# Kernel optimization log

Measured on AMD Instinct MI355X. Metric: run time of the kernel, lower is better.

The kernel has to match this reference:

```python
import jax, jax.numpy as jnp
import numpy as np

GRID = 8          # proto_grid
EPS = 1e-4        # safe_norm eps
TAU = 20.0        # temperature used throughout


def avg_pool(x, k):
    # non-overlapping avg pool, kernel k divides H and W exactly
    S, C, H, W = x.shape
    return x.reshape(S, C, H // k, k, W // k, k).mean(axis=(3, 5))


def safe_norm(x, axis):
    n = jnp.sqrt(jnp.sum(x * x, axis=axis, keepdims=True))
    return x / jnp.maximum(n, EPS)


def setup_inputs() -> dict:
    key = jax.random.key(0)
    k1, k2, k3 = jax.random.split(key, 3)
    qry = jax.random.normal(k1, (1, 1, 256, 128, 128), dtype=jnp.float32)
    sup_x = jax.random.normal(k2, (1, 5, 1, 256, 128, 128), dtype=jnp.float32)
    sup_y = jax.random.uniform(k3, (1, 5, 1, 128, 128), dtype=jnp.float32)
    return {"qry": qry, "sup_x": sup_x, "sup_y": sup_y, "thresh": 0}


def reference(qry, sup_x, sup_y, thresh):
    # mode == 'gridconv', use_cross_attn=False, isval=False
    qry = qry[:, 0]          # squeeze(1)        -> [1, 256, 128, 128]
    sup_x = sup_x[0, :, 0]   # squeeze(0,2)      -> [5, 256, 128, 128]
    sup_y = sup_y[0]         # squeeze(0)        -> [5, 1, 128, 128]

    shot, nc, H, W = sup_x.shape
    k = H // GRID

    # grid prototypes: avgpool then [shot, nc, g*g] -> [shot, g*g, nc] -> [shot*g*g, nc]
    n_sup = avg_pool(sup_x, k)
    protos = n_sup.reshape(shot, nc, -1).transpose(0, 2, 1).reshape(-1, nc)
    # selection mask: avg_pool(sup_y) > thresh. sup_y is uniform(0,1) and
    # thresh=0, so every grid cell is selected -> selection is the identity
    # (fixed-shape, jit-safe; matches the torch boolean index exactly here).

    # mean-center then safe L2-normalize (channel dim)
    protos = protos - protos.mean(axis=-1, keepdims=True)
    qryc = qry - qry.mean(axis=1, keepdims=True)
    pro_n = safe_norm(protos, axis=1)        # [npro, nc]
    qry_n = safe_norm(qryc, axis=1)          # [b, nc, h, w]

    # 1x1 conv as cosine similarity against prototype bank
    dists = jnp.einsum('bchw,pc->bphw', qry_n, pro_n) * TAU   # [b, npro, h, w]
    prob = jax.nn.softmax(dists, axis=1)
    # bmm combine: channel-wise weighted prototypes per pixel
    ch_proto = jnp.einsum('pc,bphw->bchw', pro_n, prob)       # [b, nc, h, w]
    pred_grid = jnp.sum(qry_n * ch_proto * TAU, axis=1, keepdims=True)

    debug_assign = jnp.argmax(dists, axis=1).astype(jnp.float32)
    return pred_grid, debug_assign
```

## Files before the change

### kernel.cpp

```cpp
#include <hip/hip_runtime.h>

#define NCH   256
#define NPROT 320
#define HW    16384
#define TAU   20.0f
#define EPSN  1e-4f

__global__ __launch_bounds__(256) void k_pool(const float* __restrict__ sup_x,
                                              float* __restrict__ praw) {
    int b = blockIdx.x;
    int t = threadIdx.x;
    const float4* plane = (const float4*)(sup_x + (size_t)b * HW);
    float rsum[8];
    #pragma unroll
    for (int r = 0; r < 8; ++r) rsum[r] = 0.f;
    #pragma unroll
    for (int i = 0; i < 16; ++i) {
        float4 v = plane[i * 256 + t];
        rsum[i >> 1] += v.x + v.y + v.z + v.w;
    }
    __shared__ float part[8][256];
    #pragma unroll
    for (int r = 0; r < 8; ++r) part[r][t] = rsum[r];
    __syncthreads();
    int R  = t >> 5;
    int cw = t & 31;
    float s = 0.f;
    #pragma unroll
    for (int a = 0; a < 8; ++a) s += part[R][a * 32 + cw];
    s += __shfl_xor(s, 1);
    s += __shfl_xor(s, 2);
    if ((t & 3) == 0) {
        int shot = b >> 8, c = b & 255;
        int p = shot * 64 + R * 8 + (cw >> 2);
        praw[(size_t)p * NCH + c] = s * (1.0f / 256.0f);
    }
}

__device__ __forceinline__ float block_sum256(float x, float* ws4, int t) {
    #pragma unroll
    for (int o = 1; o < 64; o <<= 1) x += __shfl_xor(x, o);
    if ((t & 63) == 0) ws4[t >> 6] = x;
    __syncthreads();
    float r = ws4[0] + ws4[1] + ws4[2] + ws4[3];
    __syncthreads();
    return r;
}

__global__ __launch_bounds__(256) void k_norm(const float* __restrict__ praw,
                                              float* __restrict__ PT,
                                              float* __restrict__ sp) {
    int p = blockIdx.x;
    int c = threadIdx.x;
    __shared__ float ws4[4];
    float v = praw[p * NCH + c];
    float mean = block_sum256(v, ws4, c) * (1.0f / 256.0f);
    float cen = v - mean;
    float n2 = block_sum256(cen * cen, ws4, c);
    float inv = 1.0f / fmaxf(sqrtf(n2), EPSN);
    float pn = cen * inv;
    PT[(size_t)(c >> 2) * NPROT * 4 + p * 4 + (c & 3)] = pn;
    float ssum = block_sum256(pn, ws4, c);
    if (c == 0) sp[p] = ssum;
}

__global__ __launch_bounds__(256, 2) void k_main(const float* __restrict__ qry,
                                                 const float* __restrict__ PT,
                                                 const float* __restrict__ sp,
                                                 float* __restrict__ out) {
    __shared__ __align__(16) float smem[9472];
    __shared__ float meanv[32], invnv[32];
    int t = threadIdx.x;
    int pixbase = blockIdx.x * 32;

    {
        int f4 = t & 7;
        int c0 = t >> 3;
        #pragma unroll
        for (int i = 0; i < 8; ++i) {
            int c = c0 + 32 * i;
            float4 v = *(const float4*)(qry + (size_t)c * HW + pixbase + f4 * 4);
            int px = f4 * 4;
            smem[(px + 0) * 260 + c] = v.x;
            smem[(px + 1) * 260 + c] = v.y;
            smem[(px + 2) * 260 + c] = v.z;
            smem[(px + 3) * 260 + c] = v.w;
        }
    }
    __syncthreads();

    {
        int pix = t & 31, sub = t >> 5;
        float s1 = 0.f, s2 = 0.f;
        #pragma unroll
        for (int j = 0; j < 32; ++j) {
            float q = smem[pix * 260 + sub * 32 + j];
            s1 += q; s2 += q * q;
        }
        smem[8320 + sub * 32 + pix] = s1;
        smem[8576 + sub * 32 + pix] = s2;
    }
    __syncthreads();
    if (t < 32) {
        float s1 = 0.f, s2 = 0.f;
        #pragma unroll
        for (int j = 0; j < 8; ++j) { s1 += smem[8320 + j * 32 + t]; s2 += smem[8576 + j * 32 + t]; }
        float mean = s1 * (1.0f / 256.0f);
        float n2 = fmaxf(s2 - s1 * mean, 0.f);
        meanv[t] = mean;
        invnv[t] = 1.0f / fmaxf(sqrtf(n2), EPSN);
    }
    __syncthreads();

    int lane = t & 63;
    int w = t >> 6;
    float acc[8][5];
    #pragma unroll
    for (int i = 0; i < 8; ++i)
        #pragma unroll
        for (int j = 0; j < 5; ++j) acc[i][j] = 0.f;

    {
        const float4* pptr = (const float4*)PT + lane;
        const float* qbase = smem + w * 8 * 260;
        for (int cb = 0; cb < 64; ++cb) {
            float4 pv0 = pptr[0];
            float4 pv1 = pptr[64];
            float4 pv2 = pptr[128];
            float4 pv3 = pptr[192];
            float4 pv4 = pptr[256];
            #pragma unroll
            for (int i = 0; i < 8; ++i) {
                float4 qv = *(const float4*)(qbase + i * 260);
                acc[i][0] = fmaf(qv.x, pv0.x, acc[i][0]);
                acc[i][0] = fmaf(qv.y, pv0.y, acc[i][0]);
                acc[i][0] = fmaf(qv.z, pv0.z, acc[i][0]);
                acc[i][0] = fmaf(qv.w, pv0.w, acc[i][0]);
                acc[i][1] = fmaf(qv.x, pv1.x, acc[i][1]);
                acc[i][1] = fmaf(qv.y, pv1.y, acc[i][1]);
                acc[i][1] = fmaf(qv.z, pv1.z, acc[i][1]);
                acc[i][1] = fmaf(qv.w, pv1.w, acc[i][1]);
                acc[i][2] = fmaf(qv.x, pv2.x, acc[i][2]);
                acc[i][2] = fmaf(qv.y, pv2.y, acc[i][2]);
                acc[i][2] = fmaf(qv.z, pv2.z, acc[i][2]);
                acc[i][2] = fmaf(qv.w, pv2.w, acc[i][2]);
                acc[i][3] = fmaf(qv.x, pv3.x, acc[i][3]);
                acc[i][3] = fmaf(qv.y, pv3.y, acc[i][3]);
                acc[i][3] = fmaf(qv.z, pv3.z, acc[i][3]);
                acc[i][3] = fmaf(qv.w, pv3.w, acc[i][3]);
                acc[i][4] = fmaf(qv.x, pv4.x, acc[i][4]);
                acc[i][4] = fmaf(qv.y, pv4.y, acc[i][4]);
                acc[i][4] = fmaf(qv.z, pv4.z, acc[i][4]);
                acc[i][4] = fmaf(qv.w, pv4.w, acc[i][4]);
            }
            pptr += NPROT;
            qbase += 4;
        }
    }

    float spv[5];
    #pragma unroll
    for (int j = 0; j < 5; ++j) spv[j] = sp[lane + 64 * j];

    float m8[8], S8[8], T8[8], I8[8];
    #pragma unroll
    for (int i = 0; i < 8; ++i) {
        int pix = w * 8 + i;
        float mean = meanv[pix], invn = invnv[pix];
        float d[5];
        float m = -1e30f; int bj = 0;
        #pragma unroll
        for (int j = 0; j < 5; ++j) {
            d[j] = TAU * invn * (acc[i][j] - mean * spv[j]);
            if (d[j] > m) { m = d[j]; bj = j; }
        }
        float S = 0.f, T = 0.f;
        #pragma unroll
        for (int j = 0; j < 5; ++j) {
            float e = __expf(d[j] - m);
            S += e; T += e * d[j];
        }
        m8[i] = m; S8[i] = S; T8[i] = T; I8[i] = (float)(lane + 64 * bj);
    }
    __syncthreads();

    float* M  = smem;
    float* Sa = smem + 2080;
    float* Ta = smem + 4160;
    float* Ia = smem + 6240;
    #pragma unroll
    for (int i = 0; i < 8; ++i) {
        int pix = w * 8 + i;
        M [pix * 65 + lane] = m8[i];
        Sa[pix * 65 + lane] = S8[i];
        Ta[pix * 65 + lane] = T8[i];
        Ia[pix * 65 + lane] = I8[i];
    }
    __syncthreads();

    float* P2m = smem + 8320;
    float* P2s = smem + 8608;
    float* P2t = smem + 8896;
    float* P2i = smem + 9184;
    {
        int pix = t >> 3, oct = t & 7;
        int base = pix * 65 + oct * 8;
        float gm = -1e30f;
        #pragma unroll
        for (int k = 0; k < 8; ++k) gm = fmaxf(gm, M[base + k]);
        float S = 0.f, T = 0.f, bi = 0.f, bm = -1e30f;
        #pragma unroll
        for (int k = 0; k < 8; ++k) {
            float mk = M[base + k];
            float wg = __expf(mk - gm);
            S += Sa[base + k] * wg;
            T += Ta[base + k] * wg;
            if (mk > bm) { bm = mk; bi = Ia[base + k]; }
        }
        P2m[pix * 9 + oct] = gm;
        P2s[pix * 9 + oct] = S;
        P2t[pix * 9 + oct] = T;
        P2i[pix * 9 + oct] = bi;
    }
    __syncthreads();

    if (t < 32) {
        float gm = -1e30f;
        #pragma unroll
        for (int k = 0; k < 8; ++k) gm = fmaxf(gm, P2m[t * 9 + k]);
        float S = 0.f, T = 0.f, bi = 0.f, bm = -1e30f;
        #pragma unroll
        for (int k = 0; k < 8; ++k) {
            float mk = P2m[t * 9 + k];
            float wg = __expf(mk - gm);
            S += P2s[t * 9 + k] * wg;
            T += P2t[t * 9 + k] * wg;
            if (mk > bm) { bm = mk; bi = P2i[t * 9 + k]; }
        }
        out[pixbase + t] = T / S;
        out[HW + pixbase + t] = bi;
    }
}

extern "C" void kernel_launch(void* const* d_in, const int* in_sizes, int n_in,
                              void* d_out, int out_size, void* d_ws, size_t ws_size,
                              hipStream_t stream) {
    const float* qry   = (const float*)d_in[0];
    const float* sup_x = (const float*)d_in[1];
    float* out = (float*)d_out;

    float* praw = (float*)d_ws;
    float* PT   = praw + NPROT * NCH;
    float* sp   = PT + NPROT * NCH;

    k_pool<<<5 * 256, 256, 0, stream>>>(sup_x, praw);
    k_norm<<<NPROT, 256, 0, stream>>>(praw, PT, sp);
    k_main<<<HW / 32, 256, 0, stream>>>(qry, PT, sp, out);
}
```

Measured before the change: 192.9 us.

## Compute prototype similarity with split-fp16 MFMA instead of scalar FP32 FMAs

Moves the query-prototype dot product from scalar FP32 FMA loops onto 16x16x32 fp16 MFMA instructions. Both operands are split into fp16 hi and scaled lo parts, and three MFMA products recover near-FP32 accuracy. Queries are normalized and split in LDS with an XOR swizzle, and prototypes are stored pre-split in k_norm, so the sum-of-prototype correction term goes away. The softmax/argmax reduction is restructured around the MFMA output layout using shuffles and a smaller cross-wave combine. This adds conversion work and LDS usage, and risks small precision differences.

```diff
diff --git a/kernel.cpp b/kernel.cpp
--- a/kernel.cpp
+++ b/kernel.cpp
@@ -5,6 +5,9 @@
 #define HW    16384
 #define TAU   20.0f
 #define EPSN  1e-4f
+
+typedef _Float16 half8 __attribute__((ext_vector_type(8)));
+typedef float    f32x4 __attribute__((ext_vector_type(4)));
 
 __global__ __launch_bounds__(256) void k_pool(const float* __restrict__ sup_x,
                                               float* __restrict__ praw) {
@@ -48,8 +51,8 @@
 }
 
 __global__ __launch_bounds__(256) void k_norm(const float* __restrict__ praw,
-                                              float* __restrict__ PT,
-                                              float* __restrict__ sp) {
+                                              _Float16* __restrict__ PTh,
+                                              _Float16* __restrict__ PTl) {
     int p = blockIdx.x;
     int c = threadIdx.x;
     __shared__ float ws4[4];
@@ -59,17 +62,23 @@
     float n2 = block_sum256(cen * cen, ws4, c);
     float inv = 1.0f / fmaxf(sqrtf(n2), EPSN);
     float pn = cen * inv;
-    PT[(size_t)(c >> 2) * NPROT * 4 + p * 4 + (c & 3)] = pn;
-    float ssum = block_sum256(pn, ws4, c);
-    if (c == 0) sp[p] = ssum;
+    _Float16 hi = (_Float16)pn;
+    float lo = (pn - (float)hi) * 2048.0f;
+    size_t idx = ((size_t)(c >> 3) * NPROT + p) * 8 + (c & 7);
+    PTh[idx] = hi;
+    PTl[idx] = (_Float16)lo;
 }
 
 __global__ __launch_bounds__(256, 2) void k_main(const float* __restrict__ qry,
-                                                 const float* __restrict__ PT,
-                                                 const float* __restrict__ sp,
+                                                 const _Float16* __restrict__ PTh,
+                                                 const _Float16* __restrict__ PTl,
                                                  float* __restrict__ out) {
-    __shared__ __align__(16) float smem[9472];
+    __shared__ __align__(16) float qlds[32 * 260];
+    __shared__ float red[512];
+    __shared__ __align__(16) _Float16 Ah[32 * 256];
+    __shared__ __align__(16) _Float16 Al[32 * 256];
     __shared__ float meanv[32], invnv[32];
+    __shared__ float Mw[4][32], Sw[4][32], Tw[4][32], Iw[4][32];
     int t = threadIdx.x;
     int pixbase = blockIdx.x * 32;
 
@@ -81,10 +90,10 @@
             int c = c0 + 32 * i;
             float4 v = *(const float4*)(qry + (size_t)c * HW + pixbase + f4 * 4);
             int px = f4 * 4;
-            smem[(px + 0) * 260 + c] = v.x;
-            smem[(px + 1) * 260 + c] = v.y;
-            smem[(px + 2) * 260 + c] = v.z;
-            smem[(px + 3) * 260 + c] = v.w;
+            qlds[(px + 0) * 260 + c] = v.x;
+            qlds[(px + 1) * 260 + c] = v.y;
+            qlds[(px + 2) * 260 + c] = v.z;
+            qlds[(px + 3) * 260 + c] = v.w;
         }
     }
     __syncthreads();
@@ -94,17 +103,17 @@
         float s1 = 0.f, s2 = 0.f;
         #pragma unroll
         for (int j = 0; j < 32; ++j) {
-            float q = smem[pix * 260 + sub * 32 + j];
+            float q = qlds[pix * 260 + sub * 32 + j];
             s1 += q; s2 += q * q;
         }
-        smem[8320 + sub * 32 + pix] = s1;
-        smem[8576 + sub * 32 + pix] = s2;
+        red[sub * 32 + pix] = s1;
+        red[256 + sub * 32 + pix] = s2;
     }
     __syncthreads();
     if (t < 32) {
         float s1 = 0.f, s2 = 0.f;
         #pragma unroll
-        for (int j = 0; j < 8; ++j) { s1 += smem[8320 + j * 32 + t]; s2 += smem[8576 + j * 32 + t]; }
+        for (int j = 0; j < 8; ++j) { s1 += red[j * 32 + t]; s2 += red[256 + j * 32 + t]; }
         float mean = s1 * (1.0f / 256.0f);
         float n2 = fmaxf(s2 - s1 * mean, 0.f);
         meanv[t] = mean;
@@ -112,133 +121,121 @@
     }
     __syncthreads();
 
-    int lane = t & 63;
-    int w = t >> 6;
-    float acc[8][5];
-    #pragma unroll
-    for (int i = 0; i < 8; ++i)
-        #pragma unroll
-        for (int j = 0; j < 5; ++j) acc[i][j] = 0.f;
-
-    {
-        const float4* pptr = (const float4*)PT + lane;
-        const float* qbase = smem + w * 8 * 260;
-        for (int cb = 0; cb < 64; ++cb) {
-            float4 pv0 = pptr[0];
-            float4 pv1 = pptr[64];
-            float4 pv2 = pptr[128];
-            float4 pv3 = pptr[192];
-            float4 pv4 = pptr[256];
-            #pragma unroll
-            for (int i = 0; i < 8; ++i) {
-                float4 qv = *(const float4*)(qbase + i * 260);
-                acc[i][0] = fmaf(qv.x, pv0.x, acc[i][0]);
-                acc[i][0] = fmaf(qv.y, pv0.y, acc[i][0]);
-                acc[i][0] = fmaf(qv.z, pv0.z, acc[i][0]);
-                acc[i][0] = fmaf(qv.w, pv0.w, acc[i][0]);
-                acc[i][1] = fmaf(qv.x, pv1.x, acc[i][1]);
-                acc[i][1] = fmaf(qv.y, pv1.y, acc[i][1]);
-                acc[i][1] = fmaf(qv.z, pv1.z, acc[i][1]);
-                acc[i][1] = fmaf(qv.w, pv1.w, acc[i][1]);
-                acc[i][2] = fmaf(qv.x, pv2.x, acc[i][2]);
-                acc[i][2] = fmaf(qv.y, pv2.y, acc[i][2]);
-                acc[i][2] = fmaf(qv.z, pv2.z, acc[i][2]);
-                acc[i][2] = fmaf(qv.w, pv2.w, acc[i][2]);
-                acc[i][3] = fmaf(qv.x, pv3.x, acc[i][3]);
-                acc[i][3] = fmaf(qv.y, pv3.y, acc[i][3]);
-                acc[i][3] = fmaf(qv.z, pv3.z, acc[i][3]);
-                acc[i][3] = fmaf(qv.w, pv3.w, acc[i][3]);
-                acc[i][4] = fmaf(qv.x, pv4.x, acc[i][4]);
-                acc[i][4] = fmaf(qv.y, pv4.y, acc[i][4]);
-                acc[i][4] = fmaf(qv.z, pv4.z, acc[i][4]);
-                acc[i][4] = fmaf(qv.w, pv4.w, acc[i][4]);
-            }
-            pptr += NPROT;
-            qbase += 4;
-        }
-    }
-
-    float spv[5];
-    #pragma unroll
-    for (int j = 0; j < 5; ++j) spv[j] = sp[lane + 64 * j];
-
-    float m8[8], S8[8], T8[8], I8[8];
-    #pragma unroll
-    for (int i = 0; i < 8; ++i) {
-        int pix = w * 8 + i;
-        float mean = meanv[pix], invn = invnv[pix];
-        float d[5];
-        float m = -1e30f; int bj = 0;
-        #pragma unroll
-        for (int j = 0; j < 5; ++j) {
-            d[j] = TAU * invn * (acc[i][j] - mean * spv[j]);
-            if (d[j] > m) { m = d[j]; bj = j; }
-        }
+    {
+        int px = t >> 3, g = t & 7;
+        float mean = meanv[px], invn = invnv[px];
+        #pragma unroll
+        for (int c8 = 0; c8 < 4; ++c8) {
+            int k0 = g * 32 + c8 * 8;
+            const float* src = &qlds[px * 260 + k0];
+            half8 hv, lv;
+            #pragma unroll
+            for (int j = 0; j < 8; ++j) {
+                float qn = (src[j] - mean) * invn;
+                _Float16 h = (_Float16)qn;
+                hv[j] = h;
+                lv[j] = (_Float16)((qn - (float)h) * 2048.0f);
+            }
+            int off = px * 512 + ((k0 * 2) ^ ((px & 7) << 4));
+            *(half8*)((char*)Ah + off) = hv;
+            *(half8*)((char*)Al + off) = lv;
+        }
+    }
+    __syncthreads();
+
+    int lane = t & 63, w = t >> 6;
+    int col = lane & 15, g4 = lane >> 4;
+
+    f32x4 acc1[2][5], acc2[2][5];
+    #pragma unroll
+    for (int mt = 0; mt < 2; ++mt)
+        #pragma unroll
+        for (int nt = 0; nt < 5; ++nt) {
+            acc1[mt][nt] = (f32x4){0.f, 0.f, 0.f, 0.f};
+            acc2[mt][nt] = (f32x4){0.f, 0.f, 0.f, 0.f};
+        }
+
+    {
+        const half8* BH = (const half8*)PTh;
+        const half8* BL = (const half8*)PTl;
+        int nb = w * 80 + col;
+        int aswz = (col & 7) << 4;
+        const char* AhB = (const char*)Ah + col * 512;
+        const char* AlB = (const char*)Al + col * 512;
+        #pragma unroll
+        for (int kb = 0; kb < 8; ++kb) {
+            int rowb = (kb * 4 + g4) * 320 + nb;
+            half8 bh[5], bl[5];
+            #pragma unroll
+            for (int nt = 0; nt < 5; ++nt) {
+                bh[nt] = BH[rowb + nt * 16];
+                bl[nt] = BL[rowb + nt * 16];
+            }
+            int koff = (kb * 64 + g4 * 16) ^ aswz;
+            half8 ah0 = *(const half8*)(AhB + koff);
+            half8 ah1 = *(const half8*)(AhB + koff + 8192);
+            half8 al0 = *(const half8*)(AlB + koff);
+            half8 al1 = *(const half8*)(AlB + koff + 8192);
+            #pragma unroll
+            for (int nt = 0; nt < 5; ++nt) {
+                acc1[0][nt] = __builtin_amdgcn_mfma_f32_16x16x32_f16(ah0, bh[nt], acc1[0][nt], 0, 0, 0);
+                acc1[1][nt] = __builtin_amdgcn_mfma_f32_16x16x32_f16(ah1, bh[nt], acc1[1][nt], 0, 0, 0);
+                acc2[0][nt] = __builtin_amdgcn_mfma_f32_16x16x32_f16(ah0, bl[nt], acc2[0][nt], 0, 0, 0);
+                acc2[0][nt] = __builtin_amdgcn_mfma_f32_16x16x32_f16(al0, bh[nt], acc2[0][nt], 0, 0, 0);
+                acc2[1][nt] = __builtin_amdgcn_mfma_f32_16x16x32_f16(ah1, bl[nt], acc2[1][nt], 0, 0, 0);
+                acc2[1][nt] = __builtin_amdgcn_mfma_f32_16x16x32_f16(al1, bh[nt], acc2[1][nt], 0, 0, 0);
+            }
+        }
+    }
+
+    #pragma unroll
+    for (int mt = 0; mt < 2; ++mt) {
+        #pragma unroll
+        for (int r = 0; r < 4; ++r) {
+            int pixel = mt * 16 + g4 * 4 + r;
+            float dv[5];
+            #pragma unroll
+            for (int nt = 0; nt < 5; ++nt)
+                dv[nt] = TAU * (acc1[mt][nt][r] + acc2[mt][nt][r] * (1.0f / 2048.0f));
+            float gm = dv[0];
+            float gi = (float)(w * 80 + col);
+            #pragma unroll
+            for (int nt = 1; nt < 5; ++nt)
+                if (dv[nt] > gm) { gm = dv[nt]; gi = (float)(w * 80 + nt * 16 + col); }
+            #pragma unroll
+            for (int o = 1; o < 16; o <<= 1) {
+                float om = __shfl_xor(gm, o);
+                float oi = __shfl_xor(gi, o);
+                if (om > gm || (om == gm && oi < gi)) { gm = om; gi = oi; }
+            }
+            float S = 0.f, T = 0.f;
+            #pragma unroll
+            for (int nt = 0; nt < 5; ++nt) {
+                float e = __expf(dv[nt] - gm);
+                S += e;
+                T = fmaf(e, dv[nt], T);
+            }
+            #pragma unroll
+            for (int o = 1; o < 16; o <<= 1) { S += __shfl_xor(S, o); T += __shfl_xor(T, o); }
+            if (col == 0) { Mw[w][pixel] = gm; Sw[w][pixel] = S; Tw[w][pixel] = T; Iw[w][pixel] = gi; }
+        }
+    }
+    __syncthreads();
+
+    if (t < 32) {
+        float gm = Mw[0][t], gi = Iw[0][t];
+        #pragma unroll
+        for (int k = 1; k < 4; ++k)
+            if (Mw[k][t] > gm) { gm = Mw[k][t]; gi = Iw[k][t]; }
         float S = 0.f, T = 0.f;
         #pragma unroll
-        for (int j = 0; j < 5; ++j) {
-            float e = __expf(d[j] - m);
-            S += e; T += e * d[j];
-        }
-        m8[i] = m; S8[i] = S; T8[i] = T; I8[i] = (float)(lane + 64 * bj);
-    }
-    __syncthreads();
-
-    float* M  = smem;
-    float* Sa = smem + 2080;
-    float* Ta = smem + 4160;
-    float* Ia = smem + 6240;
-    #pragma unroll
-    for (int i = 0; i < 8; ++i) {
-        int pix = w * 8 + i;
-        M [pix * 65 + lane] = m8[i];
-        Sa[pix * 65 + lane] = S8[i];
-        Ta[pix * 65 + lane] = T8[i];
-        Ia[pix * 65 + lane] = I8[i];
-    }
-    __syncthreads();
-
-    float* P2m = smem + 8320;
-    float* P2s = smem + 8608;
-    float* P2t = smem + 8896;
-    float* P2i = smem + 9184;
-    {
-        int pix = t >> 3, oct = t & 7;
-        int base = pix * 65 + oct * 8;
-        float gm = -1e30f;
-        #pragma unroll
-        for (int k = 0; k < 8; ++k) gm = fmaxf(gm, M[base + k]);
-        float S = 0.f, T = 0.f, bi = 0.f, bm = -1e30f;
-        #pragma unroll
-        for (int k = 0; k < 8; ++k) {
-            float mk = M[base + k];
-            float wg = __expf(mk - gm);
-            S += Sa[base + k] * wg;
-            T += Ta[base + k] * wg;
-            if (mk > bm) { bm = mk; bi = Ia[base + k]; }
-        }
-        P2m[pix * 9 + oct] = gm;
-        P2s[pix * 9 + oct] = S;
-        P2t[pix * 9 + oct] = T;
-        P2i[pix * 9 + oct] = bi;
-    }
-    __syncthreads();
-
-    if (t < 32) {
-        float gm = -1e30f;
-        #pragma unroll
-        for (int k = 0; k < 8; ++k) gm = fmaxf(gm, P2m[t * 9 + k]);
-        float S = 0.f, T = 0.f, bi = 0.f, bm = -1e30f;
-        #pragma unroll
-        for (int k = 0; k < 8; ++k) {
-            float mk = P2m[t * 9 + k];
-            float wg = __expf(mk - gm);
-            S += P2s[t * 9 + k] * wg;
-            T += P2t[t * 9 + k] * wg;
-            if (mk > bm) { bm = mk; bi = P2i[t * 9 + k]; }
+        for (int k = 0; k < 4; ++k) {
+            float sc = __expf(Mw[k][t] - gm);
+            S = fmaf(Sw[k][t], sc, S);
+            T = fmaf(Tw[k][t], sc, T);
         }
         out[pixbase + t] = T / S;
-        out[HW + pixbase + t] = bi;
+        out[HW + pixbase + t] = gi;
     }
 }
 
@@ -249,11 +246,11 @@
     const float* sup_x = (const float*)d_in[1];
     float* out = (float*)d_out;
 
-    float* praw = (float*)d_ws;
-    float* PT   = praw + NPROT * NCH;
-    float* sp   = PT + NPROT * NCH;
+    float* praw   = (float*)d_ws;
+    _Float16* PTh = (_Float16*)(praw + NPROT * NCH);
+    _Float16* PTl = PTh + NPROT * NCH;
 
     k_pool<<<5 * 256, 256, 0, stream>>>(sup_x, praw);
-    k_norm<<<NPROT, 256, 0, stream>>>(praw, PT, sp);
-    k_main<<<HW / 32, 256, 0, stream>>>(qry, PT, sp, out);
-}
+    k_norm<<<NPROT, 256, 0, stream>>>(praw, PTh, PTl);
+    k_main<<<HW / 32, 256, 0, stream>>>(qry, PTh, PTl, out);
+}
```

Measured after the change: 159.5 us. 17.4% less time.
